# Kernel tuning notes

Hardware: AMD Instinct MI355X
Metric: run time of the kernel (lower is better)

Reference implementation:

```python
import jax, jax.numpy as jnp
import numpy as np

D_MODEL = 256
N = 8192

def setup_inputs() -> dict:
    key = jax.random.key(0)
    k1, k2, k3, k4 = jax.random.split(key, 4)
    x = jax.random.normal(k1, (N, D_MODEL), dtype=jnp.float32)
    # nn.Linear weights: shape [out, in], applied as x @ W.T
    s = 1.0 / np.sqrt(D_MODEL)
    Wq = jax.random.normal(k2, (D_MODEL, D_MODEL), dtype=jnp.float32) * s
    Wk = jax.random.normal(k3, (D_MODEL, D_MODEL), dtype=jnp.float32) * s
    Wv = jax.random.normal(k4, (D_MODEL, D_MODEL), dtype=jnp.float32) * s
    return {"x": x, "Wq": Wq, "Wk": Wk, "Wv": Wv}

def reference(x, Wq, Wk, Wv):
    d_model = Wq.shape[0]
    Q = x @ Wq.T  # [N, d]
    K = x @ Wk.T
    V = x @ Wv.T
    scores = (Q @ K.T) / jnp.sqrt(jnp.asarray(d_model, x.dtype))  # [N, N]
    attn = jax.nn.softmax(scores, axis=-1)  # stable max-sub softmax, same math
    cntx = attn @ V  # [N, d]
    return (cntx, attn)
```

## Files before the change

kernel.cpp:

```cpp
#include <hip/hip_runtime.h>

#define D_MODEL 256
#define NSEQ    8192
#define PV_GROUPS 4

typedef _Float16 half8 __attribute__((ext_vector_type(8)));
typedef _Float16 half4 __attribute__((ext_vector_type(4)));
typedef float    f32x4 __attribute__((ext_vector_type(4)));

__device__ __forceinline__ half8 cvt8(f32x4 a, f32x4 b) {
  half8 h;
  h[0]=(_Float16)a[0]; h[1]=(_Float16)a[1]; h[2]=(_Float16)a[2]; h[3]=(_Float16)a[3];
  h[4]=(_Float16)b[0]; h[5]=(_Float16)b[1]; h[6]=(_Float16)b[2]; h[7]=(_Float16)b[3];
  return h;
}

__device__ __forceinline__ half8 load8_f32(const float* p) {
  f32x4 a = *(const f32x4*)p;
  f32x4 b = *(const f32x4*)(p + 4);
  return cvt8(a, b);
}

__global__ __launch_bounds__(256) void qkv_kernel(
    const float* __restrict__ x, const float* __restrict__ Wq,
    const float* __restrict__ Wk, const float* __restrict__ Wv,
    _Float16* __restrict__ QK16, _Float16* __restrict__ VT)
{
  const int tid  = threadIdx.x;
  const int lane = tid & 63;
  const int wave = tid >> 6;
  const int c    = lane & 15;
  const int quad = lane >> 4;
  const int M0   = blockIdx.x * 128 + (wave >> 1) * 64;
  const int Nblk = blockIdx.y * 128 + (wave & 1) * 64;
  const int widx = Nblk >> 8;
  const int nloc = Nblk & 255;
  const float* W = (widx == 0) ? Wq : (widx == 1 ? Wk : Wv);

  f32x4 acc[4][4] = {};
  for (int k0 = 0; k0 < D_MODEL; k0 += 32) {
    half8 af[4], bf[4];
#pragma unroll
    for (int mt = 0; mt < 4; ++mt)
      af[mt] = load8_f32(&x[(size_t)(M0 + mt*16 + c) * D_MODEL + k0 + quad*8]);
#pragma unroll
    for (int nt = 0; nt < 4; ++nt)
      bf[nt] = load8_f32(&W[(size_t)(nloc + nt*16 + c) * D_MODEL + k0 + quad*8]);
#pragma unroll
    for (int mt = 0; mt < 4; ++mt)
#pragma unroll
      for (int nt = 0; nt < 4; ++nt)
        acc[mt][nt] = __builtin_amdgcn_mfma_f32_16x16x32_f16(af[mt], bf[nt], acc[mt][nt], 0, 0, 0);
  }

  if (widx < 2) {
#pragma unroll
    for (int mt = 0; mt < 4; ++mt)
#pragma unroll
      for (int nt = 0; nt < 4; ++nt) {
        const int col  = widx * 256 + nloc + nt*16 + c;
        const int row0 = M0 + mt*16 + quad*4;
#pragma unroll
        for (int r = 0; r < 4; ++r)
          QK16[(size_t)(row0 + r) * 512 + col] = (_Float16)acc[mt][nt][r];
      }
  } else {
#pragma unroll
    for (int mt = 0; mt < 4; ++mt)
#pragma unroll
      for (int nt = 0; nt < 4; ++nt) {
        const int d  = nloc + nt*16 + c;
        const int m0 = M0 + mt*16 + quad*4;
        half4 h;
        h[0]=(_Float16)acc[mt][nt][0]; h[1]=(_Float16)acc[mt][nt][1];
        h[2]=(_Float16)acc[mt][nt][2]; h[3]=(_Float16)acc[mt][nt][3];
        *(half4*)&VT[(size_t)d * NSEQ + m0] = h;
      }
  }
}

__global__ __launch_bounds__(256) void score_kernel(
    const _Float16* __restrict__ QK16, float* __restrict__ S,
    float* __restrict__ lsum)
{
  const int tid  = threadIdx.x;
  const int lane = tid & 63;
  const int wave = tid >> 6;
  const int c    = lane & 15;
  const int quad = lane >> 4;
  const int M0   = blockIdx.x * 128 + (wave >> 1) * 64;
  const int N0   = blockIdx.y * 128 + (wave & 1) * 64;

  f32x4 acc[4][4] = {};
  for (int k0 = 0; k0 < 256; k0 += 32) {
    half8 af[4], bf[4];
#pragma unroll
    for (int mt = 0; mt < 4; ++mt)
      af[mt] = *(const half8*)&QK16[(size_t)(M0 + mt*16 + c) * 512 + k0 + quad*8];
#pragma unroll
    for (int nt = 0; nt < 4; ++nt)
      bf[nt] = *(const half8*)&QK16[(size_t)(N0 + nt*16 + c) * 512 + 256 + k0 + quad*8];
#pragma unroll
    for (int mt = 0; mt < 4; ++mt)
#pragma unroll
      for (int nt = 0; nt < 4; ++nt)
        acc[mt][nt] = __builtin_amdgcn_mfma_f32_16x16x32_f16(af[mt], bf[nt], acc[mt][nt], 0, 0, 0);
  }

  float psum[4][4] = {};
#pragma unroll
  for (int mt = 0; mt < 4; ++mt)
#pragma unroll
    for (int nt = 0; nt < 4; ++nt)
#pragma unroll
      for (int r = 0; r < 4; ++r) {
        const float p = __expf(acc[mt][nt][r] * 0.0625f);
        psum[mt][r] += p;
        S[(size_t)(M0 + mt*16 + quad*4 + r) * NSEQ + N0 + nt*16 + c] = p;
      }

#pragma unroll
  for (int mt = 0; mt < 4; ++mt)
#pragma unroll
    for (int r = 0; r < 4; ++r) {
      float v = psum[mt][r];
      v += __shfl_xor(v, 1);
      v += __shfl_xor(v, 2);
      v += __shfl_xor(v, 4);
      v += __shfl_xor(v, 8);
      if (c == 0) atomicAdd(&lsum[M0 + mt*16 + quad*4 + r], v);
    }
}

__global__ __launch_bounds__(256) void pv_kernel(
    float* __restrict__ attn, const float* __restrict__ lsum,
    const _Float16* __restrict__ VT, float* __restrict__ cntx)
{
  __shared__ _Float16 As[64 * 40];
  __shared__ float linv[64];
  const int tid  = threadIdx.x;
  const int lane = tid & 63;
  const int wave = tid >> 6;
  const int c    = lane & 15;
  const int quad = lane >> 4;
  const int M0   = blockIdx.x * 64;
  const int jb   = blockIdx.y * (NSEQ / PV_GROUPS);
  const int je   = jb + NSEQ / PV_GROUPS;
  const int D0   = wave * 64;
  const int sr   = tid >> 2;
  const int sc   = (tid & 3) * 8;

  if (tid < 64) linv[tid] = 1.0f / lsum[M0 + tid];
  __syncthreads();

  f32x4 acc[4][4] = {};
  for (int j0 = jb; j0 < je; j0 += 32) {
    float* prow = &attn[(size_t)(M0 + sr) * NSEQ + j0 + sc];
    f32x4 p0 = *(f32x4*)prow;
    f32x4 p1 = *(f32x4*)(prow + 4);
    const float s = linv[sr];
    p0 = p0 * s;
    p1 = p1 * s;
    *(f32x4*)prow       = p0;
    *(f32x4*)(prow + 4) = p1;
    __syncthreads();
    *(half8*)&As[sr * 40 + sc] = cvt8(p0, p1);
    __syncthreads();

    half8 af[4], bf[4];
#pragma unroll
    for (int mt = 0; mt < 4; ++mt)
      af[mt] = *(const half8*)&As[(mt*16 + c) * 40 + quad*8];
#pragma unroll
    for (int nt = 0; nt < 4; ++nt)
      bf[nt] = *(const half8*)&VT[(size_t)(D0 + nt*16 + c) * NSEQ + j0 + quad*8];
#pragma unroll
    for (int mt = 0; mt < 4; ++mt)
#pragma unroll
      for (int nt = 0; nt < 4; ++nt)
        acc[mt][nt] = __builtin_amdgcn_mfma_f32_16x16x32_f16(af[mt], bf[nt], acc[mt][nt], 0, 0, 0);
  }

#pragma unroll
  for (int mt = 0; mt < 4; ++mt)
#pragma unroll
    for (int nt = 0; nt < 4; ++nt)
#pragma unroll
      for (int r = 0; r < 4; ++r)
        atomicAdd(&cntx[(size_t)(M0 + mt*16 + quad*4 + r) * D_MODEL + D0 + nt*16 + c],
                  acc[mt][nt][r]);
}

extern "C" void kernel_launch(void* const* d_in, const int* in_sizes, int n_in,
                              void* d_out, int out_size, void* d_ws, size_t ws_size,
                              hipStream_t stream)
{
  const float* x  = (const float*)d_in[0];
  const float* Wq = (const float*)d_in[1];
  const float* Wk = (const float*)d_in[2];
  const float* Wv = (const float*)d_in[3];

  float* cntx = (float*)d_out;
  float* attn = cntx + (size_t)NSEQ * D_MODEL;

  _Float16* QK16 = (_Float16*)d_ws;
  _Float16* VT   = QK16 + (size_t)NSEQ * 512;
  float*    lsum = (float*)(VT + (size_t)D_MODEL * NSEQ);

  hipMemsetAsync(cntx, 0, sizeof(float) * (size_t)NSEQ * D_MODEL, stream);
  hipMemsetAsync(lsum, 0, sizeof(float) * NSEQ, stream);

  qkv_kernel<<<dim3(64, 6), 256, 0, stream>>>(x, Wq, Wk, Wv, QK16, VT);
  score_kernel<<<dim3(64, 64), 256, 0, stream>>>(QK16, attn, lsum);
  pv_kernel<<<dim3(128, PV_GROUPS), 256, 0, stream>>>(attn, lsum, VT, cntx);
}
```

Baseline: 604.0 us.

## Fuse QK^T exp with PV accumulation and recompute scores for normalized attn output

```diff
diff --git a/kernel.cpp b/kernel.cpp
--- a/kernel.cpp
+++ b/kernel.cpp
@@ -2,7 +2,7 @@
 
 #define D_MODEL 256
 #define NSEQ    8192
-#define PV_GROUPS 4
+#define JG      8
 
 typedef _Float16 half8 __attribute__((ext_vector_type(8)));
 typedef _Float16 half4 __attribute__((ext_vector_type(4)));
@@ -79,45 +79,71 @@
   }
 }
 
-__global__ __launch_bounds__(256) void score_kernel(
-    const _Float16* __restrict__ QK16, float* __restrict__ S,
-    float* __restrict__ lsum)
-{
+#define PSTRIDE 136
+
+__global__ __launch_bounds__(256) void fused_pv_kernel(
+    const _Float16* __restrict__ QK16, const _Float16* __restrict__ VT,
+    float* __restrict__ lsum, float* __restrict__ cntx)
+{
+  __shared__ _Float16 Ps[64 * PSTRIDE];
   const int tid  = threadIdx.x;
   const int lane = tid & 63;
   const int wave = tid >> 6;
   const int c    = lane & 15;
   const int quad = lane >> 4;
-  const int M0   = blockIdx.x * 128 + (wave >> 1) * 64;
-  const int N0   = blockIdx.y * 128 + (wave & 1) * 64;
-
-  f32x4 acc[4][4] = {};
-  for (int k0 = 0; k0 < 256; k0 += 32) {
-    half8 af[4], bf[4];
-#pragma unroll
-    for (int mt = 0; mt < 4; ++mt)
-      af[mt] = *(const half8*)&QK16[(size_t)(M0 + mt*16 + c) * 512 + k0 + quad*8];
-#pragma unroll
-    for (int nt = 0; nt < 4; ++nt)
-      bf[nt] = *(const half8*)&QK16[(size_t)(N0 + nt*16 + c) * 512 + 256 + k0 + quad*8];
-#pragma unroll
-    for (int mt = 0; mt < 4; ++mt)
+  const int M0   = blockIdx.x * 64;
+  const int jb   = blockIdx.y * (NSEQ / JG);
+  const int je   = jb + NSEQ / JG;
+
+  f32x4 cacc[4][4] = {};
+  float psum[4][4] = {};
+
+  for (int j0 = jb; j0 < je; j0 += 128) {
+    f32x4 sacc[4][2] = {};
+    for (int k0 = 0; k0 < 256; k0 += 32) {
+      half8 af[4], bf[2];
+#pragma unroll
+      for (int mt = 0; mt < 4; ++mt)
+        af[mt] = *(const half8*)&QK16[(size_t)(M0 + mt*16 + c) * 512 + k0 + quad*8];
+#pragma unroll
+      for (int nt = 0; nt < 2; ++nt)
+        bf[nt] = *(const half8*)&QK16[(size_t)(j0 + wave*32 + nt*16 + c) * 512 + 256 + k0 + quad*8];
+#pragma unroll
+      for (int mt = 0; mt < 4; ++mt)
+#pragma unroll
+        for (int nt = 0; nt < 2; ++nt)
+          sacc[mt][nt] = __builtin_amdgcn_mfma_f32_16x16x32_f16(af[mt], bf[nt], sacc[mt][nt], 0, 0, 0);
+    }
+
+    __syncthreads();
+#pragma unroll
+    for (int mt = 0; mt < 4; ++mt)
+#pragma unroll
+      for (int nt = 0; nt < 2; ++nt)
+#pragma unroll
+        for (int r = 0; r < 4; ++r) {
+          const float p = __expf(sacc[mt][nt][r] * 0.0625f);
+          psum[mt][r] += p;
+          Ps[(mt*16 + quad*4 + r) * PSTRIDE + wave*32 + nt*16 + c] = (_Float16)p;
+        }
+    __syncthreads();
+
+#pragma unroll
+    for (int kk = 0; kk < 128; kk += 32) {
+      half8 af[4], bf[4];
+#pragma unroll
+      for (int mt = 0; mt < 4; ++mt)
+        af[mt] = *(const half8*)&Ps[(mt*16 + c) * PSTRIDE + kk + quad*8];
 #pragma unroll
       for (int nt = 0; nt < 4; ++nt)
-        acc[mt][nt] = __builtin_amdgcn_mfma_f32_16x16x32_f16(af[mt], bf[nt], acc[mt][nt], 0, 0, 0);
-  }
-
-  float psum[4][4] = {};
-#pragma unroll
-  for (int mt = 0; mt < 4; ++mt)
-#pragma unroll
-    for (int nt = 0; nt < 4; ++nt)
-#pragma unroll
-      for (int r = 0; r < 4; ++r) {
-        const float p = __expf(acc[mt][nt][r] * 0.0625f);
-        psum[mt][r] += p;
-        S[(size_t)(M0 + mt*16 + quad*4 + r) * NSEQ + N0 + nt*16 + c] = p;
-      }
+        bf[nt] = *(const half8*)&VT[(size_t)(wave*64 + nt*16 + c) * NSEQ + j0 + kk + quad*8];
+#pragma unroll
+      for (int mt = 0; mt < 4; ++mt)
+#pragma unroll
+        for (int nt = 0; nt < 4; ++nt)
+          cacc[mt][nt] = __builtin_amdgcn_mfma_f32_16x16x32_f16(af[mt], bf[nt], cacc[mt][nt], 0, 0, 0);
+    }
+  }
 
 #pragma unroll
   for (int mt = 0; mt < 4; ++mt)
@@ -130,50 +156,55 @@
       v += __shfl_xor(v, 8);
       if (c == 0) atomicAdd(&lsum[M0 + mt*16 + quad*4 + r], v);
     }
-}
-
-__global__ __launch_bounds__(256) void pv_kernel(
-    float* __restrict__ attn, const float* __restrict__ lsum,
-    const _Float16* __restrict__ VT, float* __restrict__ cntx)
-{
-  __shared__ _Float16 As[64 * 40];
-  __shared__ float linv[64];
+
+#pragma unroll
+  for (int mt = 0; mt < 4; ++mt)
+#pragma unroll
+    for (int nt = 0; nt < 4; ++nt)
+#pragma unroll
+      for (int r = 0; r < 4; ++r)
+        atomicAdd(&cntx[(size_t)(M0 + mt*16 + quad*4 + r) * D_MODEL + wave*64 + nt*16 + c],
+                  cacc[mt][nt][r]);
+}
+
+__global__ __launch_bounds__(256) void scale_cntx_kernel(
+    float* __restrict__ cntx, const float* __restrict__ lsum)
+{
+  const int g   = blockIdx.x * 256 + threadIdx.x;
+  const int row = g >> 6;
+  const float s = 1.0f / lsum[row];
+  f32x4 v = ((f32x4*)cntx)[g];
+  ((f32x4*)cntx)[g] = v * s;
+}
+
+__global__ __launch_bounds__(256) void attn_kernel(
+    const _Float16* __restrict__ QK16, const float* __restrict__ lsum,
+    float* __restrict__ attn)
+{
   const int tid  = threadIdx.x;
   const int lane = tid & 63;
   const int wave = tid >> 6;
   const int c    = lane & 15;
   const int quad = lane >> 4;
-  const int M0   = blockIdx.x * 64;
-  const int jb   = blockIdx.y * (NSEQ / PV_GROUPS);
-  const int je   = jb + NSEQ / PV_GROUPS;
-  const int D0   = wave * 64;
-  const int sr   = tid >> 2;
-  const int sc   = (tid & 3) * 8;
-
-  if (tid < 64) linv[tid] = 1.0f / lsum[M0 + tid];
-  __syncthreads();
+  const int M0   = blockIdx.x * 128 + (wave >> 1) * 64;
+  const int N0   = blockIdx.y * 128 + (wave & 1) * 64;
+
+  float linv[4][4];
+#pragma unroll
+  for (int mt = 0; mt < 4; ++mt)
+#pragma unroll
+    for (int r = 0; r < 4; ++r)
+      linv[mt][r] = 1.0f / lsum[M0 + mt*16 + quad*4 + r];
 
   f32x4 acc[4][4] = {};
-  for (int j0 = jb; j0 < je; j0 += 32) {
-    float* prow = &attn[(size_t)(M0 + sr) * NSEQ + j0 + sc];
-    f32x4 p0 = *(f32x4*)prow;
-    f32x4 p1 = *(f32x4*)(prow + 4);
-    const float s = linv[sr];
-    p0 = p0 * s;
-    p1 = p1 * s;
-    *(f32x4*)prow       = p0;
-    *(f32x4*)(prow + 4) = p1;
-    __syncthreads();
-    *(half8*)&As[sr * 40 + sc] = cvt8(p0, p1);
-    __syncthreads();
-
+  for (int k0 = 0; k0 < 256; k0 += 32) {
     half8 af[4], bf[4];
 #pragma unroll
     for (int mt = 0; mt < 4; ++mt)
-      af[mt] = *(const half8*)&As[(mt*16 + c) * 40 + quad*8];
-#pragma unroll
-    for (int nt = 0; nt < 4; ++nt)
-      bf[nt] = *(const half8*)&VT[(size_t)(D0 + nt*16 + c) * NSEQ + j0 + quad*8];
+      af[mt] = *(const half8*)&QK16[(size_t)(M0 + mt*16 + c) * 512 + k0 + quad*8];
+#pragma unroll
+    for (int nt = 0; nt < 4; ++nt)
+      bf[nt] = *(const half8*)&QK16[(size_t)(N0 + nt*16 + c) * 512 + 256 + k0 + quad*8];
 #pragma unroll
     for (int mt = 0; mt < 4; ++mt)
 #pragma unroll
@@ -187,8 +218,8 @@
     for (int nt = 0; nt < 4; ++nt)
 #pragma unroll
       for (int r = 0; r < 4; ++r)
-        atomicAdd(&cntx[(size_t)(M0 + mt*16 + quad*4 + r) * D_MODEL + D0 + nt*16 + c],
-                  acc[mt][nt][r]);
+        attn[(size_t)(M0 + mt*16 + quad*4 + r) * NSEQ + N0 + nt*16 + c] =
+            __expf(acc[mt][nt][r] * 0.0625f) * linv[mt][r];
 }
 
 extern "C" void kernel_launch(void* const* d_in, const int* in_sizes, int n_in,
@@ -211,6 +242,7 @@
   hipMemsetAsync(lsum, 0, sizeof(float) * NSEQ, stream);
 
   qkv_kernel<<<dim3(64, 6), 256, 0, stream>>>(x, Wq, Wk, Wv, QK16, VT);
-  score_kernel<<<dim3(64, 64), 256, 0, stream>>>(QK16, attn, lsum);
-  pv_kernel<<<dim3(128, PV_GROUPS), 256, 0, stream>>>(attn, lsum, VT, cntx);
-}
+  fused_pv_kernel<<<dim3(NSEQ / 64, JG), 256, 0, stream>>>(QK16, VT, lsum, cntx);
+  scale_cntx_kernel<<<dim3(2048), 256, 0, stream>>>(cntx, lsum);
+  attn_kernel<<<dim3(64, 64), 256, 0, stream>>>(QK16, lsum, attn);
+}
```

After: 616.6 us. 1.02x slower.
